# Performance work log

Measured on AMD Instinct MI355X. Metric: run time of the kernel, lower is better.

Reference implementation:

```python
import jax, jax.numpy as jnp
import numpy as np

IN_DIM = 2048
OUT_DIM = 2048
GRID_SIZE = 8
BATCH = 4096
LN_EPS = 1e-5


def setup_inputs() -> dict:
    key = jax.random.key(0)
    k_x, k_w = jax.random.split(key)
    x = jax.random.normal(k_x, (BATCH, IN_DIM), dtype=jnp.float32)
    spline_weight = jax.random.normal(k_w, (OUT_DIM, IN_DIM, GRID_SIZE), dtype=jnp.float32) * 0.1
    return {
        "x": x,
        "ln_weight": jnp.ones((IN_DIM,), jnp.float32),
        "ln_bias": jnp.zeros((IN_DIM,), jnp.float32),
        "spline_weight": spline_weight,
        "scale_base": jnp.ones((OUT_DIM, IN_DIM), jnp.float32),
        "bias": jnp.zeros((OUT_DIM,), jnp.float32),
        "rbf_beta": jnp.full((1,), 2.0, jnp.float32),
        "grid": jnp.linspace(-1.0, 1.0, GRID_SIZE, dtype=jnp.float32),
    }


def reference(x, ln_weight, ln_bias, spline_weight, scale_base, bias, rbf_beta, grid):
    # LayerNorm over last dim (eps=1e-5, elementwise affine)
    mu = jnp.mean(x, axis=-1, keepdims=True)
    var = jnp.mean(jnp.square(x - mu), axis=-1, keepdims=True)
    xn = (x - mu) * jax.lax.rsqrt(var + LN_EPS) * ln_weight + ln_bias  # (B, in)

    beta = jnp.clip(rbf_beta, 0.5, 6.0)  # (1,)
    # RBF basis: (B, in, G)
    basis = jnp.exp(-jnp.square(xn[..., None] - grid) * beta)

    # Torch einsum('bdig,oid->bod') broadcasts the singleton d of basis against
    # spline_weight's last axis and sums g; after .sum(-1) this equals
    # (sum_g basis) @ (sum_d spline_weight).T
    S = basis.sum(-1)              # (B, in)
    Wd = spline_weight.sum(-1)     # (out, in)
    spline_sum = jnp.einsum('bi,oi->bo', S, Wd)

    base_out = jnp.einsum('bi,oi->bo', xn, scale_base)
    return base_out + spline_sum + bias
```

## Files before the change

### kernel.cpp

```cpp
#include <hip/hip_runtime.h>
#include <hip/hip_bf16.h>
#include <stdint.h>

constexpr int IN_DIM   = 2048;
constexpr int OUT_DIM  = 2048;
constexpr int BATCH    = 4096;
constexpr int KDIM     = 2 * IN_DIM;
constexpr float LN_EPS = 1e-5f;

#define TILE 128
#define BK   64
constexpr int NK    = KDIM / BK;
constexpr int STAGE = TILE * BK;

typedef __attribute__((ext_vector_type(8))) short  short8;
typedef __attribute__((ext_vector_type(4))) float  f32x4;

__device__ __forceinline__ unsigned short f2bf(float f) {
  __hip_bfloat16 h = __float2bfloat16(f);
  return *reinterpret_cast<unsigned short*>(&h);
}
__device__ __forceinline__ unsigned pack2bf(float a, float b) {
  return (unsigned)f2bf(a) | ((unsigned)f2bf(b) << 16);
}

constexpr int SW_F4   = OUT_DIM * IN_DIM * 2;
constexpr int SB_F4   = OUT_DIM * IN_DIM / 4;
constexpr int PACK_BLOCKS = (SW_F4 + SB_F4) / 256;

__global__ __launch_bounds__(256) void prep_kernel(
    const float* __restrict__ x, const float* __restrict__ lnw,
    const float* __restrict__ lnb, const float* __restrict__ betap,
    const float* __restrict__ grid, unsigned short* __restrict__ A,
    const float* __restrict__ sw, const float* __restrict__ sb,
    unsigned* __restrict__ Bu)
{
  const int tid = threadIdx.x;
  if (blockIdx.x < BATCH) {
    const int row = blockIdx.x;
    const float4* xr = reinterpret_cast<const float4*>(x + (size_t)row * IN_DIM);
    float4 v0 = xr[tid];
    float4 v1 = xr[tid + 256];
    float s = (v0.x + v0.y) + (v0.z + v0.w) + (v1.x + v1.y) + (v1.z + v1.w);
    float q = v0.x * v0.x + v0.y * v0.y + v0.z * v0.z + v0.w * v0.w
            + v1.x * v1.x + v1.y * v1.y + v1.z * v1.z + v1.w * v1.w;
    #pragma unroll
    for (int off = 32; off > 0; off >>= 1) {
      s += __shfl_down(s, off, 64);
      q += __shfl_down(q, off, 64);
    }
    __shared__ float red[10];
    const int lane = tid & 63, wv = tid >> 6;
    if (lane == 0) { red[wv] = s; red[4 + wv] = q; }
    __syncthreads();
    if (tid == 0) {
      float ts = (red[0] + red[1]) + (red[2] + red[3]);
      float tq = (red[4] + red[5]) + (red[6] + red[7]);
      float mu  = ts * (1.0f / IN_DIM);
      float var = tq * (1.0f / IN_DIM) - mu * mu;
      red[8] = mu;
      red[9] = rsqrtf(var + LN_EPS);
    }
    __syncthreads();
    const float mu = red[8], rs = red[9];
    const float beta = fminf(fmaxf(betap[0], 0.5f), 6.0f);
    float g[8];
    #pragma unroll
    for (int i = 0; i < 8; i++) g[i] = grid[i];
    const float4* w4 = reinterpret_cast<const float4*>(lnw);
    const float4* b4 = reinterpret_cast<const float4*>(lnb);
    unsigned short* Ar = A + (size_t)row * KDIM;
    #pragma unroll
    for (int h = 0; h < 2; h++) {
      const int idx = tid + h * 256;
      float4 xv  = (h == 0) ? v0 : v1;
      float4 wv4 = w4[idx];
      float4 bv4 = b4[idx];
      float xa[4] = {xv.x, xv.y, xv.z, xv.w};
      float wa[4] = {wv4.x, wv4.y, wv4.z, wv4.w};
      float ba[4] = {bv4.x, bv4.y, bv4.z, bv4.w};
      float xn[4], S[4];
      #pragma unroll
      for (int c = 0; c < 4; c++) {
        float xnv = (xa[c] - mu) * rs * wa[c] + ba[c];
        xn[c] = xnv;
        float acc = 0.f;
        #pragma unroll
        for (int gg = 0; gg < 8; gg++) {
          float d = xnv - g[gg];
          acc += __expf(-beta * d * d);
        }
        S[c] = acc;
      }
      uint2 px, ps;
      px.x = pack2bf(xn[0], xn[1]);
      px.y = pack2bf(xn[2], xn[3]);
      ps.x = pack2bf(S[0], S[1]);
      ps.y = pack2bf(S[2], S[3]);
      *reinterpret_cast<uint2*>(Ar + idx * 4) = px;
      *reinterpret_cast<uint2*>(Ar + IN_DIM + idx * 4) = ps;
    }
  } else {
    const int g = (blockIdx.x - BATCH) * 256 + tid;
    const int lane = tid & 63;
    if (g < SW_F4) {
      float4 v = reinterpret_cast<const float4*>(sw)[g];
      float s = (v.x + v.y) + (v.z + v.w);
      s += __shfl_xor(s, 1, 64);
      float hi = __shfl_down(s, 2, 64);
      if ((lane & 3) == 0) {
        const int i_lin = g >> 1;
        const int o = i_lin >> 11;
        const int i = i_lin & (IN_DIM - 1);
        Bu[(size_t)o * (KDIM / 2) + (IN_DIM / 2) + (i >> 1)] = pack2bf(s, hi);
      }
    } else {
      const int t = g - SW_F4;
      float4 v = reinterpret_cast<const float4*>(sb)[t];
      const int o  = t >> 9;
      const int i4 = t & 511;
      uint2 u;
      u.x = pack2bf(v.x, v.y);
      u.y = pack2bf(v.z, v.w);
      *reinterpret_cast<uint2*>(&Bu[(size_t)o * (KDIM / 2) + i4 * 2]) = u;
    }
  }
}

__device__ __forceinline__ void gld_lds16(const unsigned short* g, unsigned short* l) {
  __builtin_amdgcn_global_load_lds(
      (const __attribute__((address_space(1))) void*)g,
      (__attribute__((address_space(3))) void*)l, 16, 0, 0);
}

__global__ __launch_bounds__(256) void gemm_kernel(
    const unsigned short* __restrict__ A, const unsigned short* __restrict__ Bm,
    const float* __restrict__ bias, float* __restrict__ out)
{
  __shared__ __align__(16) unsigned short As[2 * STAGE];
  __shared__ __align__(16) unsigned short Bs[2 * STAGE];
  const int tid  = threadIdx.x;
  const int lane = tid & 63;
  const int wv   = tid >> 6;
  const int wr   = wv >> 1;
  const int wc   = wv & 1;
  const int gid = blockIdx.x;
  const int sq  = gid & 7;
  const int q   = gid >> 3;
  const int m0  = ((sq >> 1) * 8 + (q >> 3)) * TILE;
  const int n0  = ((sq & 1) * 8 + (q & 7)) * TILE;
  const int lrow = lane & 15;
  const int lkq  = lane >> 4;

  f32x4 acc[4][4] = {};

  const unsigned short* Ap[4];
  const unsigned short* Bp[4];
  unsigned short* ldsA[4];
  unsigned short* ldsB[4];
  #pragma unroll
  for (int j = 0; j < 4; j++) {
    const int seg  = j * 256 + wv * 64 + lane;
    const int row  = seg >> 3;
    const int gcol = ((seg & 7) ^ (row & 7)) * 8;
    Ap[j] = A  + (size_t)(m0 + row) * KDIM + gcol;
    Bp[j] = Bm + (size_t)(n0 + row) * KDIM + gcol;
    ldsA[j] = &As[(j * 256 + wv * 64) * 8];
    ldsB[j] = &Bs[(j * 256 + wv * 64) * 8];
  }

  #pragma unroll
  for (int j = 0; j < 4; j++) gld_lds16(Ap[j], ldsA[j]);
  #pragma unroll
  for (int j = 0; j < 4; j++) gld_lds16(Bp[j], ldsB[j]);

  #pragma unroll 1
  for (int kt = 0; kt < NK; kt++) {
    __syncthreads();
    const int cur = (kt & 1) * STAGE;
    if (kt + 1 < NK) {
      const int nxt = ((kt + 1) & 1) * STAGE;
      const int koff = (kt + 1) * BK;
      #pragma unroll
      for (int j = 0; j < 4; j++) gld_lds16(Ap[j] + koff, ldsA[j] + nxt);
      #pragma unroll
      for (int j = 0; j < 4; j++) gld_lds16(Bp[j] + koff, ldsB[j] + nxt);
    }

    short8 af[2][4], bf[2][4];
    #pragma unroll
    for (int h = 0; h < 2; h++) {
      #pragma unroll
      for (int mi = 0; mi < 4; mi++) {
        const int r = wr * 64 + mi * 16 + lrow;
        af[h][mi] = *reinterpret_cast<const short8*>(
            &As[cur + r * BK + (((h << 2) | lkq) ^ (lrow & 7)) * 8]);
      }
      #pragma unroll
      for (int ni = 0; ni < 4; ni++) {
        const int r = wc * 64 + ni * 16 + lrow;
        bf[h][ni] = *reinterpret_cast<const short8*>(
            &Bs[cur + r * BK + (((h << 2) | lkq) ^ (lrow & 7)) * 8]);
      }
    }
    #pragma unroll
    for (int h = 0; h < 2; h++)
      #pragma unroll
      for (int mi = 0; mi < 4; mi++)
        #pragma unroll
        for (int ni = 0; ni < 4; ni++)
          acc[mi][ni] = __builtin_amdgcn_mfma_f32_16x16x32_bf16(
              af[h][mi], bf[h][ni], acc[mi][ni], 0, 0, 0);
  }

  const int rb = (lane >> 4) * 4;
  #pragma unroll
  for (int ni = 0; ni < 4; ni++) {
    const int col = n0 + wc * 64 + ni * 16 + lrow;
    const float bv = bias[col];
    #pragma unroll
    for (int mi = 0; mi < 4; mi++) {
      const int rowm = m0 + wr * 64 + mi * 16 + rb;
      #pragma unroll
      for (int r = 0; r < 4; r++)
        out[(size_t)(rowm + r) * OUT_DIM + col] = acc[mi][ni][r] + bv;
    }
  }
}

extern "C" void kernel_launch(void* const* d_in, const int* in_sizes, int n_in,
                              void* d_out, int out_size, void* d_ws, size_t ws_size,
                              hipStream_t stream) {
  const float* x    = (const float*)d_in[0];
  const float* lnw  = (const float*)d_in[1];
  const float* lnb  = (const float*)d_in[2];
  const float* sw   = (const float*)d_in[3];
  const float* sb   = (const float*)d_in[4];
  const float* bias = (const float*)d_in[5];
  const float* beta = (const float*)d_in[6];
  const float* grid = (const float*)d_in[7];
  float* out = (float*)d_out;

  unsigned short* A = (unsigned short*)d_ws;
  unsigned short* B = A + (size_t)BATCH * KDIM;

  hipLaunchKernelGGL(prep_kernel, dim3(BATCH + PACK_BLOCKS), dim3(256), 0, stream,
                     x, lnw, lnb, beta, grid, A, sw, sb, (unsigned*)B);
  hipLaunchKernelGGL(gemm_kernel, dim3((BATCH / TILE) * (OUT_DIM / TILE)), dim3(256), 0, stream,
                     A, B, bias, out);
}
```

Measured before the change: 304.4 us.

## Enlarge GEMM tile to 256x128 with BK=32 and remapped swizzled LDS layout

```diff
diff --git a/kernel.cpp b/kernel.cpp
--- a/kernel.cpp
+++ b/kernel.cpp
@@ -8,10 +8,12 @@
 constexpr int KDIM     = 2 * IN_DIM;
 constexpr float LN_EPS = 1e-5f;
 
-#define TILE 128
-#define BK   64
+#define TM 256
+#define TN 128
+#define BK 32
 constexpr int NK    = KDIM / BK;
-constexpr int STAGE = TILE * BK;
+constexpr int ASLOT = TM * BK;
+constexpr int BSLOT = TN * BK;
 
 typedef __attribute__((ext_vector_type(8))) short  short8;
 typedef __attribute__((ext_vector_type(4))) float  f32x4;
@@ -137,90 +139,104 @@
     const unsigned short* __restrict__ A, const unsigned short* __restrict__ Bm,
     const float* __restrict__ bias, float* __restrict__ out)
 {
-  __shared__ __align__(16) unsigned short As[2 * STAGE];
-  __shared__ __align__(16) unsigned short Bs[2 * STAGE];
+  __shared__ __align__(16) unsigned short As[2 * ASLOT];
+  __shared__ __align__(16) unsigned short Bs[2 * BSLOT];
   const int tid  = threadIdx.x;
   const int lane = tid & 63;
   const int wv   = tid >> 6;
   const int wr   = wv >> 1;
   const int wc   = wv & 1;
-  const int gid = blockIdx.x;
-  const int sq  = gid & 7;
-  const int q   = gid >> 3;
-  const int m0  = ((sq >> 1) * 8 + (q >> 3)) * TILE;
-  const int n0  = ((sq & 1) * 8 + (q & 7)) * TILE;
+  const int d  = blockIdx.x;
+  const int x  = d & 7, q = d >> 3;
+  const int m0 = (((x >> 1) * 4) + (q & 3)) * TM;
+  const int n0 = (((x & 1) * 8) + (q >> 2)) * TN;
   const int lrow = lane & 15;
   const int lkq  = lane >> 4;
 
-  f32x4 acc[4][4] = {};
+  f32x4 acc[8][4] = {};
 
   const unsigned short* Ap[4];
-  const unsigned short* Bp[4];
-  unsigned short* ldsA[4];
-  unsigned short* ldsB[4];
+  const unsigned short* Bp[2];
+  unsigned aB[4], bB[2];
   #pragma unroll
   for (int j = 0; j < 4; j++) {
     const int seg  = j * 256 + wv * 64 + lane;
-    const int row  = seg >> 3;
-    const int gcol = ((seg & 7) ^ (row & 7)) * 8;
-    Ap[j] = A  + (size_t)(m0 + row) * KDIM + gcol;
-    Bp[j] = Bm + (size_t)(n0 + row) * KDIM + gcol;
-    ldsA[j] = &As[(j * 256 + wv * 64) * 8];
-    ldsB[j] = &Bs[(j * 256 + wv * 64) * 8];
-  }
-
-  #pragma unroll
-  for (int j = 0; j < 4; j++) gld_lds16(Ap[j], ldsA[j]);
-  #pragma unroll
-  for (int j = 0; j < 4; j++) gld_lds16(Bp[j], ldsB[j]);
+    const int line = seg >> 3;
+    const int gi   = (seg & 7) ^ (line & 7);
+    const int row  = line * 2 + (gi >> 2);
+    const int kg   = gi & 3;
+    Ap[j] = A + (size_t)(m0 + row) * KDIM + kg * 8;
+    aB[j] = (unsigned)((j * 256 + wv * 64) * 8);
+  }
+  #pragma unroll
+  for (int j = 0; j < 2; j++) {
+    const int seg  = j * 256 + wv * 64 + lane;
+    const int line = seg >> 3;
+    const int gi   = (seg & 7) ^ (line & 7);
+    const int row  = line * 2 + (gi >> 2);
+    const int kg   = gi & 3;
+    Bp[j] = Bm + (size_t)(n0 + row) * KDIM + kg * 8;
+    bB[j] = (unsigned)((j * 256 + wv * 64) * 8);
+  }
+
+  unsigned aOff[8], bOff[4];
+  #pragma unroll
+  for (int i = 0; i < 8; i++) {
+    const int ra = wr * 128 + i * 16 + lrow;
+    const int la = ra >> 1, ga = (ra & 1) * 4 + lkq;
+    aOff[i] = (unsigned)(la * 64 + (ga ^ (la & 7)) * 8);
+  }
+  #pragma unroll
+  for (int i = 0; i < 4; i++) {
+    const int rb = wc * 64 + i * 16 + lrow;
+    const int lb = rb >> 1, gb = (rb & 1) * 4 + lkq;
+    bOff[i] = (unsigned)(lb * 64 + (gb ^ (lb & 7)) * 8);
+  }
+
+  #pragma unroll
+  for (int j = 0; j < 4; j++) gld_lds16(Ap[j], &As[aB[j]]);
+  #pragma unroll
+  for (int j = 0; j < 2; j++) gld_lds16(Bp[j], &Bs[bB[j]]);
 
   #pragma unroll 1
   for (int kt = 0; kt < NK; kt++) {
     __syncthreads();
-    const int cur = (kt & 1) * STAGE;
+    const unsigned ca = (kt & 1) * ASLOT;
+    const unsigned cb = (kt & 1) * BSLOT;
     if (kt + 1 < NK) {
-      const int nxt = ((kt + 1) & 1) * STAGE;
+      const unsigned na = ((kt + 1) & 1) * ASLOT;
+      const unsigned nb = ((kt + 1) & 1) * BSLOT;
       const int koff = (kt + 1) * BK;
       #pragma unroll
-      for (int j = 0; j < 4; j++) gld_lds16(Ap[j] + koff, ldsA[j] + nxt);
-      #pragma unroll
-      for (int j = 0; j < 4; j++) gld_lds16(Bp[j] + koff, ldsB[j] + nxt);
-    }
-
-    short8 af[2][4], bf[2][4];
-    #pragma unroll
-    for (int h = 0; h < 2; h++) {
-      #pragma unroll
-      for (int mi = 0; mi < 4; mi++) {
-        const int r = wr * 64 + mi * 16 + lrow;
-        af[h][mi] = *reinterpret_cast<const short8*>(
-            &As[cur + r * BK + (((h << 2) | lkq) ^ (lrow & 7)) * 8]);
-      }
-      #pragma unroll
-      for (int ni = 0; ni < 4; ni++) {
-        const int r = wc * 64 + ni * 16 + lrow;
-        bf[h][ni] = *reinterpret_cast<const short8*>(
-            &Bs[cur + r * BK + (((h << 2) | lkq) ^ (lrow & 7)) * 8]);
-      }
-    }
-    #pragma unroll
-    for (int h = 0; h < 2; h++)
-      #pragma unroll
-      for (int mi = 0; mi < 4; mi++)
-        #pragma unroll
-        for (int ni = 0; ni < 4; ni++)
-          acc[mi][ni] = __builtin_amdgcn_mfma_f32_16x16x32_bf16(
-              af[h][mi], bf[h][ni], acc[mi][ni], 0, 0, 0);
-  }
-
-  const int rb = (lane >> 4) * 4;
+      for (int j = 0; j < 4; j++) gld_lds16(Ap[j] + koff, &As[na + aB[j]]);
+      #pragma unroll
+      for (int j = 0; j < 2; j++) gld_lds16(Bp[j] + koff, &Bs[nb + bB[j]]);
+    }
+
+    short8 af[8], bf[4];
+    #pragma unroll
+    for (int mi = 0; mi < 8; mi++)
+      af[mi] = *reinterpret_cast<const short8*>(&As[ca + aOff[mi]]);
+    #pragma unroll
+    for (int ni = 0; ni < 4; ni++)
+      bf[ni] = *reinterpret_cast<const short8*>(&Bs[cb + bOff[ni]]);
+
+    #pragma unroll
+    for (int mi = 0; mi < 8; mi++)
+      #pragma unroll
+      for (int ni = 0; ni < 4; ni++)
+        acc[mi][ni] = __builtin_amdgcn_mfma_f32_16x16x32_bf16(
+            af[mi], bf[ni], acc[mi][ni], 0, 0, 0);
+  }
+
+  const int rbse = (lane >> 4) * 4;
   #pragma unroll
   for (int ni = 0; ni < 4; ni++) {
     const int col = n0 + wc * 64 + ni * 16 + lrow;
     const float bv = bias[col];
     #pragma unroll
-    for (int mi = 0; mi < 4; mi++) {
-      const int rowm = m0 + wr * 64 + mi * 16 + rb;
+    for (int mi = 0; mi < 8; mi++) {
+      const int rowm = m0 + wr * 128 + mi * 16 + rbse;
       #pragma unroll
       for (int r = 0; r < 4; r++)
         out[(size_t)(rowm + r) * OUT_DIM + col] = acc[mi][ni][r] + bv;
@@ -246,6 +262,6 @@
 
   hipLaunchKernelGGL(prep_kernel, dim3(BATCH + PACK_BLOCKS), dim3(256), 0, stream,
                      x, lnw, lnb, beta, grid, A, sw, sb, (unsigned*)B);
-  hipLaunchKernelGGL(gemm_kernel, dim3((BATCH / TILE) * (OUT_DIM / TILE)), dim3(256), 0, stream,
+  hipLaunchKernelGGL(gemm_kernel, dim3((BATCH / TM) * (OUT_DIM / TN)), dim3(256), 0, stream,
                      A, B, bias, out);
 }
```

Result: slower. 357.0 us (+17.3%).

## Load B fragments directly from global into registers, bypassing LDS

Applied to the files above, without the earlier changes.

```diff
diff --git a/kernel.cpp b/kernel.cpp
--- a/kernel.cpp
+++ b/kernel.cpp
@@ -138,7 +138,6 @@
     const float* __restrict__ bias, float* __restrict__ out)
 {
   __shared__ __align__(16) unsigned short As[2 * STAGE];
-  __shared__ __align__(16) unsigned short Bs[2 * STAGE];
   const int tid  = threadIdx.x;
   const int lane = tid & 63;
   const int wv   = tid >> 6;
@@ -155,54 +154,61 @@
   f32x4 acc[4][4] = {};
 
   const unsigned short* Ap[4];
-  const unsigned short* Bp[4];
   unsigned short* ldsA[4];
-  unsigned short* ldsB[4];
   #pragma unroll
   for (int j = 0; j < 4; j++) {
     const int seg  = j * 256 + wv * 64 + lane;
     const int row  = seg >> 3;
     const int gcol = ((seg & 7) ^ (row & 7)) * 8;
-    Ap[j] = A  + (size_t)(m0 + row) * KDIM + gcol;
-    Bp[j] = Bm + (size_t)(n0 + row) * KDIM + gcol;
+    Ap[j]   = A + (size_t)(m0 + row) * KDIM + gcol;
     ldsA[j] = &As[(j * 256 + wv * 64) * 8];
-    ldsB[j] = &Bs[(j * 256 + wv * 64) * 8];
-  }
+  }
+
+  const unsigned short* Bp[2][4];
+  #pragma unroll
+  for (int h = 0; h < 2; h++)
+    #pragma unroll
+    for (int ni = 0; ni < 4; ni++) {
+      const int row = n0 + wc * 64 + ni * 16 + lrow;
+      Bp[h][ni] = Bm + (size_t)row * KDIM + h * 32 + lkq * 8;
+    }
 
   #pragma unroll
   for (int j = 0; j < 4; j++) gld_lds16(Ap[j], ldsA[j]);
-  #pragma unroll
-  for (int j = 0; j < 4; j++) gld_lds16(Bp[j], ldsB[j]);
+  short8 bcur[2][4];
+  #pragma unroll
+  for (int h = 0; h < 2; h++)
+    #pragma unroll
+    for (int ni = 0; ni < 4; ni++)
+      bcur[h][ni] = *reinterpret_cast<const short8*>(Bp[h][ni]);
 
   #pragma unroll 1
   for (int kt = 0; kt < NK; kt++) {
     __syncthreads();
     const int cur = (kt & 1) * STAGE;
-    if (kt + 1 < NK) {
-      const int nxt = ((kt + 1) & 1) * STAGE;
+    short8 bnxt[2][4];
+    const bool more = (kt + 1 < NK);
+    if (more) {
+      const int nxt  = ((kt + 1) & 1) * STAGE;
       const int koff = (kt + 1) * BK;
       #pragma unroll
       for (int j = 0; j < 4; j++) gld_lds16(Ap[j] + koff, ldsA[j] + nxt);
       #pragma unroll
-      for (int j = 0; j < 4; j++) gld_lds16(Bp[j] + koff, ldsB[j] + nxt);
-    }
-
-    short8 af[2][4], bf[2][4];
-    #pragma unroll
-    for (int h = 0; h < 2; h++) {
+      for (int h = 0; h < 2; h++)
+        #pragma unroll
+        for (int ni = 0; ni < 4; ni++)
+          bnxt[h][ni] = *reinterpret_cast<const short8*>(Bp[h][ni] + koff);
+    }
+
+    short8 af[2][4];
+    #pragma unroll
+    for (int h = 0; h < 2; h++)
       #pragma unroll
       for (int mi = 0; mi < 4; mi++) {
         const int r = wr * 64 + mi * 16 + lrow;
         af[h][mi] = *reinterpret_cast<const short8*>(
             &As[cur + r * BK + (((h << 2) | lkq) ^ (lrow & 7)) * 8]);
       }
-      #pragma unroll
-      for (int ni = 0; ni < 4; ni++) {
-        const int r = wc * 64 + ni * 16 + lrow;
-        bf[h][ni] = *reinterpret_cast<const short8*>(
-            &Bs[cur + r * BK + (((h << 2) | lkq) ^ (lrow & 7)) * 8]);
-      }
-    }
     #pragma unroll
     for (int h = 0; h < 2; h++)
       #pragma unroll
@@ -210,7 +216,15 @@
         #pragma unroll
         for (int ni = 0; ni < 4; ni++)
           acc[mi][ni] = __builtin_amdgcn_mfma_f32_16x16x32_bf16(
-              af[h][mi], bf[h][ni], acc[mi][ni], 0, 0, 0);
+              af[h][mi], bcur[h][ni], acc[mi][ni], 0, 0, 0);
+
+    if (more) {
+      #pragma unroll
+      for (int h = 0; h < 2; h++)
+        #pragma unroll
+        for (int ni = 0; ni < 4; ni++)
+          bcur[h][ni] = bnxt[h][ni];
+    }
   }
 
   const int rb = (lane >> 4) * 4;
```

New measurement: 375.4 us. +23.3%, slower.
